# Kernel tuning notes

Measured on AMD Instinct MI355X. Metric: run time of the kernel, lower is better.

Reference implementation:

```python
import jax, jax.numpy as jnp
import numpy as np

B, CIN, H, W = 16, 256, 56, 56
D, HEADS, KS, PAD, STRIDE, M = 256, 8, 3, 1, 1, 4
K = KS * KS
N = D // HEADS
# relative_indices: sum of window coords, flattened row-major, values in [0, 2*KS-2]
REL = (np.arange(KS)[:, None] + np.arange(KS)[None, :]).reshape(-1)


def setup_inputs() -> dict:
    key = jax.random.key(0)
    ks = jax.random.split(key, 7)
    return {
        "x": jax.random.normal(ks[0], (B, CIN, H, W), jnp.float32),
        "q": jax.random.normal(ks[1], (B, D, 1), jnp.float32),
        "Wk": jax.random.normal(ks[2], (D, CIN), jnp.float32) * 0.05,
        "Wv": jax.random.normal(ks[3], (D, CIN), jnp.float32) * 0.05,
        "pos_emb": jax.random.normal(ks[4], (1, 2 * KS - 1), jnp.float32),
        "Wlin": jax.random.normal(ks[5], (1, M), jnp.float32),
        "Wproj": jax.random.normal(ks[6], (D, D), jnp.float32) * 0.05,
    }


def _unfold(t):
    # torch nn.Unfold: (B,C,H,W) -> (B, C*K, L); patches feature dim ordered (C, kh, kw)
    p = jax.lax.conv_general_dilated_patches(
        t, (KS, KS), (STRIDE, STRIDE), [(PAD, PAD), (PAD, PAD)])
    b, _, ho, wo = p.shape
    return p.reshape(b, -1, ho * wo), ho, wo


def reference(x, q, Wk, Wv, pos_emb, Wlin, Wproj):
    b = x.shape[0]
    k = jnp.einsum('oc,bchw->bohw', Wk, x)  # 1x1 conv, no bias
    v = jnp.einsum('oc,bchw->bohw', Wv, x)
    ku, ho, wo = _unfold(k)
    vu, _, _ = _unfold(v)
    L = ho * wo
    ku = ku.reshape(b, HEADS, N, K, L)  # (b, h, n, k, l)
    vu = vu.reshape(b, HEADS, N, K, L)
    qh = q.reshape(b, HEADS, N)  # learned per-batch query, d=1 squeezed
    attn = jnp.einsum('bhn,bhnkl->bhlk', qh, ku)  # (b,h,l,K)
    attn = attn + pos_emb[0, REL]  # relative position bias, shape (K,)
    attn = jax.nn.softmax(attn, axis=-1)
    # repeat d(=1) -> m identical rows then Linear(m,1,no bias): equals scale by sum(Wlin)
    attn = attn * jnp.sum(Wlin)
    out = jnp.einsum('bhlk,bhnkl->bhnl', attn, vu)  # (b,h,n,l)
    out = out.reshape(b, D, ho, wo)  # fold with kernel 1 == reshape
    return jnp.einsum('oc,bchw->bohw', Wproj, out)  # 1x1 proj conv
```

## Files before the change

### kernel.cpp

```cpp
#include <hip/hip_runtime.h>

#define B_     16
#define D_     256
#define HEADS_ 8
#define N_     32
#define H_     56
#define W_     56
#define L_     3136
#define LDA_A  264

typedef short short8 __attribute__((ext_vector_type(8)));
typedef float f32x4  __attribute__((ext_vector_type(4)));

__device__ __forceinline__ unsigned short f2bf(float f) {
    union { float f; unsigned u; } c; c.f = f;
    unsigned u = c.u;
    u += 0x7fffu + ((u >> 16) & 1u);
    return (unsigned short)(u >> 16);
}

__global__ __launch_bounds__(256) void convert_w_kernel(
    const float* __restrict__ Wv, const float* __restrict__ Wproj,
    const float* __restrict__ Wk, const float* __restrict__ q,
    unsigned short* __restrict__ Wvb, unsigned short* __restrict__ Wpb,
    unsigned short* __restrict__ qtb)
{
    if (blockIdx.y < 2) {
        const float* src   = (blockIdx.y == 0) ? Wv  : Wproj;
        unsigned short* dst = (blockIdx.y == 0) ? Wvb : Wpb;
        const int i = (blockIdx.x * 256 + threadIdx.x) * 4;
        float4 v = *(const float4*)(src + i);
        uint2 o;
        o.x = (unsigned)f2bf(v.x) | ((unsigned)f2bf(v.y) << 16);
        o.y = (unsigned)f2bf(v.z) | ((unsigned)f2bf(v.w) << 16);
        *(uint2*)(dst + i) = o;
    } else {
        const int b  = blockIdx.x >> 2;
        const int h0 = (blockIdx.x & 3) * 2;
        const int c  = threadIdx.x;
#pragma unroll
        for (int hh = 0; hh < 2; ++hh) {
            const int h = h0 + hh;
            const float* qb = q  + b * D_ + h * N_;
            const float* wr = Wk + (size_t)(h * N_) * D_ + c;
            float acc = 0.f;
#pragma unroll 8
            for (int n = 0; n < N_; ++n)
                acc = fmaf(qb[n], wr[(size_t)n * D_], acc);
            qtb[((size_t)b * 16 + h) * D_ + c]     = f2bf(acc);
            qtb[((size_t)b * 16 + 8 + h) * D_ + c] = 0;
        }
    }
}

__global__ __launch_bounds__(256) void gemm_v_mfma(
    const float* __restrict__ x, const unsigned short* __restrict__ Wvb,
    const unsigned short* __restrict__ qtb,
    unsigned short* __restrict__ Vo, float* __restrict__ S)
{
    __shared__ __align__(16) unsigned short As[64 * LDA_A];

    const int t = threadIdx.x;
    const int w = t >> 6, lane = t & 63, col = lane & 15, quad = lane >> 4;
    const int wr = w >> 1, wc = w & 1;
    const int bb = blockIdx.z;
    const int d0 = blockIdx.y * 64;
    const int l0 = blockIdx.x * 64;
    const bool doS = (blockIdx.y == 0);

#pragma unroll
    for (int i = 0; i < 8; ++i) {
        const int u = t + i * 256;
        const int row = u >> 5, cu = (u & 31) * 8;
        *(uint4*)&As[row * LDA_A + cu] =
            *(const uint4*)(Wvb + (size_t)(d0 + row) * D_ + cu);
    }

    const float* xg[2];
#pragma unroll
    for (int n = 0; n < 2; ++n)
        xg[n] = x + (size_t)bb * D_ * L_ + (size_t)(quad * 8) * L_
                  + l0 + wc * 32 + n * 16 + col;
    const unsigned short* qg = qtb + ((size_t)bb * 16 + col) * D_ + quad * 8;

    f32x4 acc[2][2], accS[2];
#pragma unroll
    for (int m = 0; m < 2; ++m)
#pragma unroll
        for (int n = 0; n < 2; ++n) acc[m][n] = (f32x4){0.f, 0.f, 0.f, 0.f};
#pragma unroll
    for (int n = 0; n < 2; ++n) accS[n] = (f32x4){0.f, 0.f, 0.f, 0.f};

    float pB[2][2][8];
    uint4 pQ[2];
#pragma unroll
    for (int n = 0; n < 2; ++n)
#pragma unroll
        for (int j = 0; j < 8; ++j)
            pB[0][n][j] = xg[n][(size_t)j * L_];
    pQ[0] = *(const uint4*)qg;

    __syncthreads();

#pragma unroll
    for (int kt = 0; kt < 8; ++kt) {
        const int cur = kt & 1, nxt = cur ^ 1;
        if (kt < 7) {
#pragma unroll
            for (int n = 0; n < 2; ++n)
#pragma unroll
                for (int j = 0; j < 8; ++j)
                    pB[nxt][n][j] = xg[n][(size_t)((kt + 1) * 32 + j) * L_];
            pQ[nxt] = *(const uint4*)(qg + (kt + 1) * 32);
        }

        short8 bf[2];
#pragma unroll
        for (int n = 0; n < 2; ++n) {
            union { unsigned u[4]; short8 s; } pk;
#pragma unroll
            for (int p = 0; p < 4; ++p)
                asm("v_cvt_pk_bf16_f32 %0, %1, %2" : "=v"(pk.u[p])
                    : "v"(pB[cur][n][2 * p]), "v"(pB[cur][n][2 * p + 1]));
            bf[n] = pk.s;
        }
        short8 af[2];
#pragma unroll
        for (int m = 0; m < 2; ++m)
            af[m] = *(const short8*)&As[(wr * 32 + m * 16 + col) * LDA_A
                                        + kt * 32 + quad * 8];
        const short8 aq = *(const short8*)&pQ[cur];

#pragma unroll
        for (int m = 0; m < 2; ++m)
#pragma unroll
            for (int n = 0; n < 2; ++n)
                acc[m][n] = __builtin_amdgcn_mfma_f32_16x16x32_bf16(
                    af[m], bf[n], acc[m][n], 0, 0, 0);
#pragma unroll
        for (int n = 0; n < 2; ++n)
            accS[n] = __builtin_amdgcn_mfma_f32_16x16x32_bf16(
                aq, bf[n], accS[n], 0, 0, 0);
    }

#pragma unroll
    for (int n = 0; n < 2; ++n) {
        const int l = l0 + wc * 32 + n * 16 + col;
#pragma unroll
        for (int m = 0; m < 2; ++m) {
            const int h  = (d0 >> 5) + wr;
            const int dn = m * 16 + quad * 4;
            unsigned short ob[4];
#pragma unroll
            for (int r = 0; r < 4; ++r) ob[r] = f2bf(acc[m][n][r]);
            *(uint2*)(Vo + ((size_t)(bb * HEADS_ + h) * L_ + l) * N_ + dn) =
                *(const uint2*)ob;
        }
    }

    if (doS && quad < 2) {
#pragma unroll
        for (int n = 0; n < 2; ++n) {
            const int l = l0 + wc * 32 + n * 16 + col;
#pragma unroll
            for (int r = 0; r < 4; ++r)
                S[((size_t)bb * HEADS_ + quad * 4 + r) * L_ + l] = accS[n][r];
        }
    }
}

__global__ __launch_bounds__(256) void attend_kernel(
    const float* __restrict__ S, const unsigned short* __restrict__ Vo,
    const float* __restrict__ pos_emb, const float* __restrict__ Wlin,
    unsigned short* __restrict__ Om)
{
    __shared__ __align__(16) unsigned short Vs[600 * 32];
    __shared__ float Ss[10][58];

    const int band = blockIdx.x;
    const int bh   = blockIdx.y;
    const int y0   = band * 8;
    const int t    = threadIdx.x;

    const float* Sb = S + (size_t)bh * L_;
    for (int wi = t; wi < 580; wi += 256) {
        const int row = wi / 58, c = wi - row * 58;
        const int gr = y0 - 1 + row, gc = c - 1;
        float v = 0.f;
        if (gr >= 0 && gr < H_ && gc >= 0 && gc < W_)
            v = Sb[gr * W_ + gc];
        Ss[row][c] = v;
    }

    const unsigned short* Vbase = Vo + (size_t)bh * L_ * N_;
    for (int wi = t; wi < 2400; wi += 256) {
        const int p = wi >> 2, i = wi & 3;
        const int row = p / 60, cc = p - row * 60;
        const int gr = y0 - 1 + row, gc = cc - 1;
        uint4 v = make_uint4(0u, 0u, 0u, 0u);
        if (gr >= 0 && gr < H_ && gc >= 0 && gc < W_)
            v = *(const uint4*)(Vbase + (size_t)(gr * W_ + gc) * N_ + i * 8);
        const int sfc = wi ^ (p & 7);
        *(uint4*)(Vs + sfc * 8) = v;
    }
    __syncthreads();

    const float scale = Wlin[0] + Wlin[1] + Wlin[2] + Wlin[3];
    const float pe0 = pos_emb[0], pe1 = pos_emb[1], pe2 = pos_emb[2];
    const float pe3 = pos_emb[3], pe4 = pos_emb[4];
    const float bias[9] = {pe0, pe1, pe2, pe1, pe2, pe3, pe2, pe3, pe4};

    for (int idx = t; idx < 448; idx += 256) {
        const int yl = idx / 56, xx = idx - yl * 56;
        const int lr = yl + 1, lc = xx + 1;

        float lg[9], m = -1e30f;
#pragma unroll
        for (int dy = 0; dy < 3; ++dy)
#pragma unroll
            for (int dx = 0; dx < 3; ++dx) {
                const int k = dy * 3 + dx;
                lg[k] = Ss[lr - 1 + dy][lc - 1 + dx] + bias[k];
                m = fmaxf(m, lg[k]);
            }
        float ssum = 0.f;
#pragma unroll
        for (int k = 0; k < 9; ++k) { lg[k] = __expf(lg[k] - m); ssum += lg[k]; }
        const float inv = scale / ssum;

        float om[32];
#pragma unroll
        for (int i = 0; i < 32; ++i) om[i] = 0.f;

#pragma unroll
        for (int dy = 0; dy < 3; ++dy)
#pragma unroll
            for (int dx = 0; dx < 3; ++dx) {
                const float wk = lg[dy * 3 + dx] * inv;
                const int pos  = (lr - 1 + dy) * 60 + (lc - 1 + dx);
                const int base = pos * 4;
                const int msk  = pos & 7;
#pragma unroll
                for (int i = 0; i < 4; ++i) {
                    const int sfc = (base + i) ^ msk;
                    const uint4 v = *(const uint4*)(Vs + sfc * 8);
                    const unsigned* u = (const unsigned*)&v;
#pragma unroll
                    for (int j = 0; j < 4; ++j) {
                        union { unsigned uu; float f; } lo, hi;
                        lo.uu = u[j] << 16;
                        hi.uu = u[j] & 0xffff0000u;
                        om[i * 8 + 2 * j]     = fmaf(wk, lo.f, om[i * 8 + 2 * j]);
                        om[i * 8 + 2 * j + 1] = fmaf(wk, hi.f, om[i * 8 + 2 * j + 1]);
                    }
                }
            }

        unsigned short ob[32];
#pragma unroll
        for (int i = 0; i < 32; ++i) ob[i] = f2bf(om[i]);
        const int l = (y0 + yl) * W_ + xx;
        uint4* dst = (uint4*)(Om + ((size_t)bh * L_ + l) * N_);
        const uint4* sb = (const uint4*)ob;
#pragma unroll
        for (int i = 0; i < 4; ++i) dst[i] = sb[i];
    }
}

__global__ __launch_bounds__(256) void gemm_proj_mfma(
    const unsigned short* __restrict__ Om, const unsigned short* __restrict__ Wpb,
    float* __restrict__ Out)
{
    __shared__ __align__(16) char smem[64 * LDA_A * 2];
    unsigned short* As = (unsigned short*)smem;
    float*          Cs = (float*)smem;

    const int t = threadIdx.x;
    const int w = t >> 6, lane = t & 63, col = lane & 15, quad = lane >> 4;
    const int wr = w >> 1, wc = w & 1;
    const int bb = blockIdx.z;
    const int d0 = blockIdx.y * 64;
    const int l0 = blockIdx.x * 64;

#pragma unroll
    for (int i = 0; i < 8; ++i) {
        const int u = t + i * 256;
        const int row = u >> 5, cu = (u & 31) * 8;
        *(uint4*)&As[row * LDA_A + cu] =
            *(const uint4*)(Wpb + (size_t)(d0 + row) * D_ + cu);
    }

    const unsigned short* og[2];
#pragma unroll
    for (int n = 0; n < 2; ++n) {
        const int l = l0 + wc * 32 + n * 16 + col;
        og[n] = Om + ((size_t)(bb * HEADS_) * L_ + l) * N_ + quad * 8;
    }
    const size_t kstride = (size_t)L_ * N_;

    f32x4 acc[2][2];
#pragma unroll
    for (int m = 0; m < 2; ++m)
#pragma unroll
        for (int n = 0; n < 2; ++n) acc[m][n] = (f32x4){0.f, 0.f, 0.f, 0.f};

    uint4 pB[2][2];
#pragma unroll
    for (int n = 0; n < 2; ++n) pB[0][n] = *(const uint4*)og[n];

    __syncthreads();

#pragma unroll
    for (int kt = 0; kt < 8; ++kt) {
        const int cur = kt & 1, nxt = cur ^ 1;
        if (kt < 7) {
#pragma unroll
            for (int n = 0; n < 2; ++n)
                pB[nxt][n] = *(const uint4*)(og[n] + (size_t)(kt + 1) * kstride);
        }
        short8 af[2];
#pragma unroll
        for (int m = 0; m < 2; ++m)
            af[m] = *(const short8*)&As[(wr * 32 + m * 16 + col) * LDA_A
                                        + kt * 32 + quad * 8];
#pragma unroll
        for (int m = 0; m < 2; ++m)
#pragma unroll
            for (int n = 0; n < 2; ++n)
                acc[m][n] = __builtin_amdgcn_mfma_f32_16x16x32_bf16(
                    af[m], *(const short8*)&pB[cur][n], acc[m][n], 0, 0, 0);
    }

    __syncthreads();
#pragma unroll
    for (int m = 0; m < 2; ++m)
#pragma unroll
        for (int n = 0; n < 2; ++n)
#pragma unroll
            for (int r = 0; r < 4; ++r)
                Cs[(wr * 32 + m * 16 + quad * 4 + r) * 68
                   + wc * 32 + n * 16 + col] = acc[m][n][r];
    __syncthreads();

    float* ob = Out + (size_t)bb * D_ * L_ + (size_t)d0 * L_ + l0;
#pragma unroll
    for (int i = 0; i < 4; ++i) {
        const int u = t + i * 256;
        const int row = u >> 4, lc = (u & 15) * 4;
        *(float4*)(ob + (size_t)row * L_ + lc) = *(const float4*)&Cs[row * 68 + lc];
    }
}

extern "C" void kernel_launch(void* const* d_in, const int* in_sizes, int n_in,
                              void* d_out, int out_size, void* d_ws, size_t ws_size,
                              hipStream_t stream)
{
    const float* x       = (const float*)d_in[0];
    const float* q       = (const float*)d_in[1];
    const float* Wk      = (const float*)d_in[2];
    const float* Wv      = (const float*)d_in[3];
    const float* pos_emb = (const float*)d_in[4];
    const float* Wlin    = (const float*)d_in[5];
    const float* Wproj   = (const float*)d_in[6];
    float* out = (float*)d_out;

    const size_t planeE = (size_t)B_ * D_ * L_;
    unsigned short* Vo  = (unsigned short*)d_ws;
    unsigned short* Om  = Vo + planeE;
    unsigned short* Wvb = Om + planeE;
    unsigned short* Wpb = Wvb + D_ * D_;
    float*          S   = (float*)(Wpb + D_ * D_);
    unsigned short* qtb = (unsigned short*)(S + (size_t)B_ * HEADS_ * L_);

    convert_w_kernel<<<dim3(64, 3), 256, 0, stream>>>(Wv, Wproj, Wk, q, Wvb, Wpb, qtb);
    gemm_v_mfma<<<dim3(L_ / 64, 4, B_), 256, 0, stream>>>(x, Wvb, qtb, Vo, S);
    attend_kernel<<<dim3(7, B_ * HEADS_), 256, 0, stream>>>(S, Vo, pos_emb, Wlin, Om);
    gemm_proj_mfma<<<dim3(L_ / 64, 4, B_), 256, 0, stream>>>(Om, Wpb, out);
}
```

Before: 185.5 us.

## Retile V and projection GEMMs to cover all output channels per block

Both 1x1-conv GEMMs now use 32-column spatial tiles that compute all 256 output channels per block. Before, 64x64 tiles spread over four blocks in the channel dimension, so each x column was re-read and re-converted four times. In the V GEMM, x is loaded once per block with coalesced float4 reads, converted to bf16 and staged in LDS. Weight fragments are now read straight from global/L2 instead of LDS, and register double-buffering is dropped. The projection epilogue writes through a smaller LDS buffer in four synchronized passes. Together these cut redundant activation reads and raise occupancy via launch bounds, at the cost of more weight traffic from L2 and less explicit latency hiding.

```diff
diff --git a/kernel.cpp b/kernel.cpp
--- a/kernel.cpp
+++ b/kernel.cpp
@@ -7,7 +7,6 @@
 #define H_     56
 #define W_     56
 #define L_     3136
-#define LDA_A  264
 
 typedef short short8 __attribute__((ext_vector_type(8)));
 typedef float f32x4  __attribute__((ext_vector_type(4)));
@@ -53,103 +52,84 @@
     }
 }
 
-__global__ __launch_bounds__(256) void gemm_v_mfma(
+__global__ __launch_bounds__(256, 4) void gemm_v_mfma(
     const float* __restrict__ x, const unsigned short* __restrict__ Wvb,
     const unsigned short* __restrict__ qtb,
     unsigned short* __restrict__ Vo, float* __restrict__ S)
 {
-    __shared__ __align__(16) unsigned short As[64 * LDA_A];
+    __shared__ __align__(16) unsigned short Bs[32 * 264];
+    unsigned* Bd = (unsigned*)Bs;
 
     const int t = threadIdx.x;
     const int w = t >> 6, lane = t & 63, col = lane & 15, quad = lane >> 4;
-    const int wr = w >> 1, wc = w & 1;
-    const int bb = blockIdx.z;
-    const int d0 = blockIdx.y * 64;
-    const int l0 = blockIdx.x * 64;
-    const bool doS = (blockIdx.y == 0);
-
-#pragma unroll
-    for (int i = 0; i < 8; ++i) {
-        const int u = t + i * 256;
-        const int row = u >> 5, cu = (u & 31) * 8;
-        *(uint4*)&As[row * LDA_A + cu] =
-            *(const uint4*)(Wvb + (size_t)(d0 + row) * D_ + cu);
-    }
-
-    const float* xg[2];
-#pragma unroll
-    for (int n = 0; n < 2; ++n)
-        xg[n] = x + (size_t)bb * D_ * L_ + (size_t)(quad * 8) * L_
-                  + l0 + wc * 32 + n * 16 + col;
+    const int bb = blockIdx.y;
+    const int l0 = blockIdx.x * 32;
+
+    {
+        const int lg = t & 7;
+        const int u8 = t >> 3;
+        const float* xb = x + (size_t)bb * D_ * L_ + l0 + lg * 4;
+#pragma unroll
+        for (int s = 0; s < 4; ++s) {
+            const int cp = s * 32 + ((u8 + 4 * lg) & 31);
+            const float4 a = *(const float4*)(xb + (size_t)(2 * cp) * L_);
+            const float4 b = *(const float4*)(xb + (size_t)(2 * cp + 1) * L_);
+            unsigned d[4];
+            asm("v_cvt_pk_bf16_f32 %0, %1, %2" : "=v"(d[0]) : "v"(a.x), "v"(b.x));
+            asm("v_cvt_pk_bf16_f32 %0, %1, %2" : "=v"(d[1]) : "v"(a.y), "v"(b.y));
+            asm("v_cvt_pk_bf16_f32 %0, %1, %2" : "=v"(d[2]) : "v"(a.z), "v"(b.z));
+            asm("v_cvt_pk_bf16_f32 %0, %1, %2" : "=v"(d[3]) : "v"(a.w), "v"(b.w));
+#pragma unroll
+            for (int j = 0; j < 4; ++j)
+                Bd[(lg * 4 + j) * 132 + cp] = d[j];
+        }
+    }
+
+    const unsigned short* Ag = Wvb + (size_t)(w * 64 + col) * D_ + quad * 8;
     const unsigned short* qg = qtb + ((size_t)bb * 16 + col) * D_ + quad * 8;
 
-    f32x4 acc[2][2], accS[2];
-#pragma unroll
-    for (int m = 0; m < 2; ++m)
+    f32x4 acc[4][2], accS[2];
+#pragma unroll
+    for (int m = 0; m < 4; ++m)
 #pragma unroll
         for (int n = 0; n < 2; ++n) acc[m][n] = (f32x4){0.f, 0.f, 0.f, 0.f};
 #pragma unroll
     for (int n = 0; n < 2; ++n) accS[n] = (f32x4){0.f, 0.f, 0.f, 0.f};
 
-    float pB[2][2][8];
-    uint4 pQ[2];
-#pragma unroll
-    for (int n = 0; n < 2; ++n)
-#pragma unroll
-        for (int j = 0; j < 8; ++j)
-            pB[0][n][j] = xg[n][(size_t)j * L_];
-    pQ[0] = *(const uint4*)qg;
-
     __syncthreads();
 
 #pragma unroll
     for (int kt = 0; kt < 8; ++kt) {
-        const int cur = kt & 1, nxt = cur ^ 1;
-        if (kt < 7) {
-#pragma unroll
-            for (int n = 0; n < 2; ++n)
-#pragma unroll
-                for (int j = 0; j < 8; ++j)
-                    pB[nxt][n][j] = xg[n][(size_t)((kt + 1) * 32 + j) * L_];
-            pQ[nxt] = *(const uint4*)(qg + (kt + 1) * 32);
-        }
-
+        short8 af[4];
+#pragma unroll
+        for (int m = 0; m < 4; ++m)
+            af[m] = *(const short8*)(Ag + (size_t)m * 16 * D_ + kt * 32);
         short8 bf[2];
 #pragma unroll
-        for (int n = 0; n < 2; ++n) {
-            union { unsigned u[4]; short8 s; } pk;
-#pragma unroll
-            for (int p = 0; p < 4; ++p)
-                asm("v_cvt_pk_bf16_f32 %0, %1, %2" : "=v"(pk.u[p])
-                    : "v"(pB[cur][n][2 * p]), "v"(pB[cur][n][2 * p + 1]));
-            bf[n] = pk.s;
-        }
-        short8 af[2];
-#pragma unroll
-        for (int m = 0; m < 2; ++m)
-            af[m] = *(const short8*)&As[(wr * 32 + m * 16 + col) * LDA_A
-                                        + kt * 32 + quad * 8];
-        const short8 aq = *(const short8*)&pQ[cur];
-
-#pragma unroll
-        for (int m = 0; m < 2; ++m)
+        for (int n = 0; n < 2; ++n)
+            bf[n] = *(const short8*)&Bs[(n * 16 + col) * 264 + kt * 32 + quad * 8];
+#pragma unroll
+        for (int m = 0; m < 4; ++m)
 #pragma unroll
             for (int n = 0; n < 2; ++n)
                 acc[m][n] = __builtin_amdgcn_mfma_f32_16x16x32_bf16(
                     af[m], bf[n], acc[m][n], 0, 0, 0);
-#pragma unroll
-        for (int n = 0; n < 2; ++n)
-            accS[n] = __builtin_amdgcn_mfma_f32_16x16x32_bf16(
-                aq, bf[n], accS[n], 0, 0, 0);
+        if (w == 0) {
+            const short8 aq = *(const short8*)(qg + kt * 32);
+#pragma unroll
+            for (int n = 0; n < 2; ++n)
+                accS[n] = __builtin_amdgcn_mfma_f32_16x16x32_bf16(
+                    aq, bf[n], accS[n], 0, 0, 0);
+        }
     }
 
 #pragma unroll
     for (int n = 0; n < 2; ++n) {
-        const int l = l0 + wc * 32 + n * 16 + col;
-#pragma unroll
-        for (int m = 0; m < 2; ++m) {
-            const int h  = (d0 >> 5) + wr;
-            const int dn = m * 16 + quad * 4;
+        const int l = l0 + n * 16 + col;
+#pragma unroll
+        for (int m = 0; m < 4; ++m) {
+            const int h  = w * 2 + (m >> 1);
+            const int dn = (m & 1) * 16 + quad * 4;
             unsigned short ob[4];
 #pragma unroll
             for (int r = 0; r < 4; ++r) ob[r] = f2bf(acc[m][n][r]);
@@ -158,10 +138,10 @@
         }
     }
 
-    if (doS && quad < 2) {
+    if (w == 0 && quad < 2) {
 #pragma unroll
         for (int n = 0; n < 2; ++n) {
-            const int l = l0 + wc * 32 + n * 16 + col;
+            const int l = l0 + n * 16 + col;
 #pragma unroll
             for (int r = 0; r < 4; ++r)
                 S[((size_t)bb * HEADS_ + quad * 4 + r) * L_ + l] = accS[n][r];
@@ -267,87 +247,65 @@
     }
 }
 
-__global__ __launch_bounds__(256) void gemm_proj_mfma(
+__global__ __launch_bounds__(256, 4) void gemm_proj_mfma(
     const unsigned short* __restrict__ Om, const unsigned short* __restrict__ Wpb,
     float* __restrict__ Out)
 {
-    __shared__ __align__(16) char smem[64 * LDA_A * 2];
-    unsigned short* As = (unsigned short*)smem;
-    float*          Cs = (float*)smem;
+    __shared__ __align__(16) float Cs[64 * 36];
 
     const int t = threadIdx.x;
     const int w = t >> 6, lane = t & 63, col = lane & 15, quad = lane >> 4;
-    const int wr = w >> 1, wc = w & 1;
-    const int bb = blockIdx.z;
-    const int d0 = blockIdx.y * 64;
-    const int l0 = blockIdx.x * 64;
-
-#pragma unroll
-    for (int i = 0; i < 8; ++i) {
-        const int u = t + i * 256;
-        const int row = u >> 5, cu = (u & 31) * 8;
-        *(uint4*)&As[row * LDA_A + cu] =
-            *(const uint4*)(Wpb + (size_t)(d0 + row) * D_ + cu);
-    }
-
+    const int bb = blockIdx.y;
+    const int l0 = blockIdx.x * 32;
+
+    const unsigned short* Ag = Wpb + (size_t)(w * 64 + col) * D_ + quad * 8;
     const unsigned short* og[2];
 #pragma unroll
-    for (int n = 0; n < 2; ++n) {
-        const int l = l0 + wc * 32 + n * 16 + col;
-        og[n] = Om + ((size_t)(bb * HEADS_) * L_ + l) * N_ + quad * 8;
-    }
+    for (int n = 0; n < 2; ++n)
+        og[n] = Om + ((size_t)(bb * HEADS_) * L_ + l0 + n * 16 + col) * N_ + quad * 8;
     const size_t kstride = (size_t)L_ * N_;
 
-    f32x4 acc[2][2];
-#pragma unroll
-    for (int m = 0; m < 2; ++m)
+    f32x4 acc[4][2];
+#pragma unroll
+    for (int m = 0; m < 4; ++m)
 #pragma unroll
         for (int n = 0; n < 2; ++n) acc[m][n] = (f32x4){0.f, 0.f, 0.f, 0.f};
 
-    uint4 pB[2][2];
-#pragma unroll
-    for (int n = 0; n < 2; ++n) pB[0][n] = *(const uint4*)og[n];
-
-    __syncthreads();
-
 #pragma unroll
     for (int kt = 0; kt < 8; ++kt) {
-        const int cur = kt & 1, nxt = cur ^ 1;
-        if (kt < 7) {
-#pragma unroll
-            for (int n = 0; n < 2; ++n)
-                pB[nxt][n] = *(const uint4*)(og[n] + (size_t)(kt + 1) * kstride);
-        }
-        short8 af[2];
-#pragma unroll
-        for (int m = 0; m < 2; ++m)
-            af[m] = *(const short8*)&As[(wr * 32 + m * 16 + col) * LDA_A
-                                        + kt * 32 + quad * 8];
-#pragma unroll
-        for (int m = 0; m < 2; ++m)
+        short8 af[4], bf[2];
+#pragma unroll
+        for (int m = 0; m < 4; ++m)
+            af[m] = *(const short8*)(Ag + (size_t)m * 16 * D_ + kt * 32);
+#pragma unroll
+        for (int n = 0; n < 2; ++n)
+            bf[n] = *(const short8*)(og[n] + (size_t)kt * kstride);
+#pragma unroll
+        for (int m = 0; m < 4; ++m)
 #pragma unroll
             for (int n = 0; n < 2; ++n)
                 acc[m][n] = __builtin_amdgcn_mfma_f32_16x16x32_bf16(
-                    af[m], *(const short8*)&pB[cur][n], acc[m][n], 0, 0, 0);
-    }
-
-    __syncthreads();
-#pragma unroll
-    for (int m = 0; m < 2; ++m)
+                    af[m], bf[n], acc[m][n], 0, 0, 0);
+    }
+
+#pragma unroll
+    for (int m = 0; m < 4; ++m) {
+        __syncthreads();
 #pragma unroll
         for (int n = 0; n < 2; ++n)
 #pragma unroll
             for (int r = 0; r < 4; ++r)
-                Cs[(wr * 32 + m * 16 + quad * 4 + r) * 68
-                   + wc * 32 + n * 16 + col] = acc[m][n][r];
-    __syncthreads();
-
-    float* ob = Out + (size_t)bb * D_ * L_ + (size_t)d0 * L_ + l0;
-#pragma unroll
-    for (int i = 0; i < 4; ++i) {
-        const int u = t + i * 256;
-        const int row = u >> 4, lc = (u & 15) * 4;
-        *(float4*)(ob + (size_t)row * L_ + lc) = *(const float4*)&Cs[row * 68 + lc];
+                Cs[(w * 16 + quad * 4 + r) * 36 + n * 16 + col] = acc[m][n][r];
+        __syncthreads();
+#pragma unroll
+        for (int i = 0; i < 2; ++i) {
+            const int u  = t + i * 256;
+            const int lr = u >> 3;
+            const int lc = (u & 7) * 4;
+            const int d  = (lr >> 4) * 64 + m * 16 + (lr & 15);
+            *(float4*)(Out + ((size_t)bb * D_ + d) * L_ + l0 + lc) =
+                *(const float4*)&Cs[lr * 36 + lc];
+        }
     }
 }
 
@@ -373,7 +331,7 @@
     unsigned short* qtb = (unsigned short*)(S + (size_t)B_ * HEADS_ * L_);
 
     convert_w_kernel<<<dim3(64, 3), 256, 0, stream>>>(Wv, Wproj, Wk, q, Wvb, Wpb, qtb);
-    gemm_v_mfma<<<dim3(L_ / 64, 4, B_), 256, 0, stream>>>(x, Wvb, qtb, Vo, S);
+    gemm_v_mfma<<<dim3(L_ / 32, 16), 256, 0, stream>>>(x, Wvb, qtb, Vo, S);
     attend_kernel<<<dim3(7, B_ * HEADS_), 256, 0, stream>>>(S, Vo, pos_emb, Wlin, Om);
-    gemm_proj_mfma<<<dim3(L_ / 64, 4, B_), 256, 0, stream>>>(Om, Wpb, out);
-}
+    gemm_proj_mfma<<<dim3(L_ / 32, 16), 256, 0, stream>>>(Om, Wpb, out);
+}
```

New measurement: 197.1 us. +6.2%, slower.
